# Optimization experiments

Measured on AMD Instinct MI355X. Metric: run time of the kernel, lower is better.

The kernel has to match this reference:

```python
import jax, jax.numpy as jnp
import numpy as np

KERNEL_SIZES = [2, 4, 8, 16, 32, 64]
MAXK = max(k + k // 2 for k in KERNEL_SIZES[1:])  # 96
PAD_LO = (MAXK - 1) // 2  # 47
PAD_HI = MAXK - 1 - PAD_LO  # 48


def _alternating(K, even_negative):
    f = np.ones(K, np.float32)
    idx = np.arange(K)
    mask = (idx % 2 == 0) if even_negative else (idx % 2 == 1)
    f[mask] = -1.0
    return f


def make_weight_bank():
    """Builds all 17 fixed filters, zero-padded and center-aligned into one
    (17, 1, MAXK) bank so a single 'same'-padded conv matches 17 torch convs.
    Alignment: torch pads left=(K-1)//2 for kernel K; embedding each kernel at
    offset (MAXK-1)//2 - (K-1)//2 inside a MAXK kernel padded (PAD_LO, PAD_HI)
    reproduces the identical output."""
    filters = []
    for K in KERNEL_SIZES:              # group 1: -1 at even indices
        filters.append(_alternating(K, True))
    for K in KERNEL_SIZES:              # group 2: -1 at odd indices
        filters.append(_alternating(K, False))
    for K in KERNEL_SIZES[1:]:          # group 3: piecewise quadratic, len K + K//2
        q = K // 4
        left = (np.linspace(0.0, 1.0, q + 1, dtype=np.float32)[1:]) ** 2
        right = left[::-1]
        filters.append(np.concatenate([-left, -right, 2 * left, 2 * right, -left, -right]).astype(np.float32))
    W = np.zeros((len(filters), 1, MAXK), np.float32)
    for i, f in enumerate(filters):
        K = len(f)
        o = (MAXK - 1) // 2 - (K - 1) // 2
        W[i, 0, o:o + K] = f
    return jnp.asarray(W)


def setup_inputs() -> dict:
    key = jax.random.key(0)
    x = jax.random.normal(key, (128, 1, 32768), dtype=jnp.float32)
    W = make_weight_bank()  # (17, 1, 96), fixed non-trainable filters
    return {"x": x, "W": W}


def reference(x, W):
    # x: (B, 1, L); W: (17, 1, MAXK). One cross-correlation conv = bank of 17
    # 'same'-padded conv1d filters; then ReLU.
    y = jax.lax.conv_general_dilated(
        x, W,
        window_strides=(1,),
        padding=[(PAD_LO, PAD_HI)],
        dimension_numbers=("NCH", "OIH", "NCH"),
    )
    return jax.nn.relu(y)  # (B, 17, L)
```

## Files before the change

### kernel.cpp

```cpp
#include <hip/hip_runtime.h>


#define S_LEN    32768
#define NFILT    17
#define TILE     1024
#define NTHREADS 256
#define PITCH    284
#define NCHUNK   139

constexpr int Z4_OFF  = 0;
constexpr int Z8_OFF  = Z4_OFF + TILE + 16;
constexpr int Z16_OFF = Z8_OFF + TILE + 32;
constexpr int ZTOT    = Z16_OFF + TILE + 64;

typedef float fvec4 __attribute__((ext_vector_type(4)));

template<int Qv>
__device__ __forceinline__ float bw(int i) {
    constexpr float inv = 1.0f / (float)Qv;
    const float t = (i < Qv) ? (float)(i + 1) * inv : (float)(2 * Qv - i) * inv;
    return t * t;
}

template<int Qv>
__device__ __forceinline__ float third_w(int j) {
    constexpr float inv = 1.0f / (float)Qv;
    const int seg = j / Qv;
    const int i = j - seg * Qv;
    const float t = ((seg & 1) == 0) ? (float)(i + 1) * inv : (float)(Qv - i) * inv;
    const float v = t * t;
    return (seg == 2 || seg == 3) ? 2.0f * v : -v;
}

template<int Qv>
__device__ __forceinline__ void zcalc(const float* __restrict__ xsl,
                                      float* __restrict__ Zf, int bi) {
    constexpr int OFF  = 49 - 3 * Qv;
    constexpr int A0Q  = OFF >> 2;
    constexpr int SH   = OFF & 3;
    constexpr int SPAN = 2 * Qv;
    constexpr int NW   = (SH + SPAN + 3 + 3) >> 2;
    const float4* __restrict__ xs4 =
        reinterpret_cast<const float4*>(xsl) + bi + A0Q;
    float a0 = 0.f, a1 = 0.f, a2 = 0.f, a3 = 0.f;
#pragma unroll
    for (int wi = 0; wi < NW; ++wi) {
        const float4 xw = xs4[wi];
#pragma unroll
        for (int e = 0; e < 4; ++e) {
            const int u = 4 * wi + e - SH;
            const float xv = (e == 0) ? xw.x : (e == 1) ? xw.y
                           : (e == 2) ? xw.z : xw.w;
            if (u >= 0 && u < SPAN)     a0 = fmaf(bw<Qv>(u),     xv, a0);
            if (u >= 1 && u < SPAN + 1) a1 = fmaf(bw<Qv>(u - 1), xv, a1);
            if (u >= 2 && u < SPAN + 2) a2 = fmaf(bw<Qv>(u - 2), xv, a2);
            if (u >= 3 && u < SPAN + 3) a3 = fmaf(bw<Qv>(u - 3), xv, a3);
        }
    }
    reinterpret_cast<float4*>(Zf)[bi] = make_float4(a0, a1, a2, a3);
}

template<int Qv>
__device__ __forceinline__ float4 bump_out(const float* __restrict__ Zf, int tid) {
    const float4* __restrict__ Z4 = reinterpret_cast<const float4*>(Zf);
    const float4 za = Z4[tid];
    const float4 zb = Z4[tid + (Qv >> 1)];
    const float4 zc = Z4[tid + Qv];
    float4 y;
    y.x = fmaf(2.f, zb.x, -(za.x + zc.x));
    y.y = fmaf(2.f, zb.y, -(za.y + zc.y));
    y.z = fmaf(2.f, zb.z, -(za.z + zc.z));
    y.w = fmaf(2.f, zb.w, -(za.w + zc.w));
    return y;
}

template<int Qv>
__device__ __forceinline__ float4 bump_direct(const float* __restrict__ xsl, int tid) {
    constexpr int SPAN = 6 * Qv;
    constexpr int C    = (SPAN - 1) / 2;
    constexpr int OFF  = 48 - C;
    constexpr int A0   = OFF >> 2;
    constexpr int SH   = OFF & 3;
    constexpr int NW   = (SH + SPAN + 3 + 3) >> 2;
    const float4* __restrict__ xs4 =
        reinterpret_cast<const float4*>(xsl) + tid + A0;
    float a0 = 0.f, a1 = 0.f, a2 = 0.f, a3 = 0.f;
#pragma unroll
    for (int wi = 0; wi < NW; ++wi) {
        const float4 xw = xs4[wi];
#pragma unroll
        for (int e = 0; e < 4; ++e) {
            const int u = 4 * wi + e - SH;
            const float xv = (e == 0) ? xw.x : (e == 1) ? xw.y
                           : (e == 2) ? xw.z : xw.w;
            if (u >= 0 && u < SPAN)     a0 = fmaf(third_w<Qv>(u),     xv, a0);
            if (u >= 1 && u < SPAN + 1) a1 = fmaf(third_w<Qv>(u - 1), xv, a1);
            if (u >= 2 && u < SPAN + 2) a2 = fmaf(third_w<Qv>(u - 2), xv, a2);
            if (u >= 3 && u < SPAN + 3) a3 = fmaf(third_w<Qv>(u - 3), xv, a3);
        }
    }
    return make_float4(a0, a1, a2, a3);
}

__device__ __forceinline__ void alt24_direct(const float* __restrict__ xsl, int tid,
                                             float4& o2, float4& o4) {
    const float4* __restrict__ xs4 =
        reinterpret_cast<const float4*>(xsl) + tid + 11;
    const float4 wA = xs4[0], wB = xs4[1], wC = xs4[2];
    const float s3 = wA.w, s4 = wB.x, s5 = wB.y, s6 = wB.z,
                s7 = wB.w, s8 = wC.x, s9 = wC.y;
    o2.x = s5 - s4;  o2.y = s6 - s5;  o2.z = s7 - s6;  o2.w = s8 - s7;
    o4.x = (s4 - s3) + (s6 - s5);
    o4.y = (s5 - s4) + (s7 - s6);
    o4.z = (s6 - s5) + (s8 - s7);
    o4.w = (s7 - s6) + (s9 - s8);
}

template<int K>
__device__ __forceinline__ float4 alt_acc(const float* __restrict__ Psp, int tid) {
    constexpr int H = (K - 1) / 2;
    float v[4];
#pragma unroll
    for (int r = 0; r < 4; ++r) {
        const int dn  = 48 - H + r;
        const int dn2 = dn + K;
        const float pa = Psp[(dn  & 3) * PITCH + tid + (dn  >> 2)];
        const float pb = Psp[(dn2 & 3) * PITCH + tid + (dn2 >> 2)];
        const float dd = pb - pa;
        v[r] = ((r + H) & 1) ? dd : -dd;
    }
    return make_float4(v[0], v[1], v[2], v[3]);
}

__global__ __launch_bounds__(NTHREADS, 6)
void conv_bank_kernel(const float* __restrict__ x, float* __restrict__ out) {
    __shared__ __align__(16) float xsl[1136];
    __shared__ float Psp[4 * PITCH];
    __shared__ __align__(16) float Zb[ZTOT];
    __shared__ float wtot[2];

    const int tid = threadIdx.x;
    const int bx  = blockIdx.x;
    const int ts  = bx * TILE;
    const int b   = blockIdx.y;
    const float* __restrict__ xrow = x + (size_t)b * S_LEN;

    if (bx >= 1 && bx <= 30) {
        const float4* __restrict__ g4 =
            reinterpret_cast<const float4*>(xrow) + ((ts - 48) >> 2);
        float4* __restrict__ s4 = reinterpret_cast<float4*>(xsl);
#pragma unroll
        for (int i = tid; i < 284; i += NTHREADS)
            s4[i] = (i < 281) ? g4[i] : make_float4(0.f, 0.f, 0.f, 0.f);
    } else {
        for (int j = tid; j < 1136; j += NTHREADS) {
            const int g = ts - 48 + j;
            xsl[j] = (j < 1124 && (unsigned)g < (unsigned)S_LEN) ? xrow[g] : 0.f;
        }
    }
    __syncthreads();

    float4 xa, xb;
    float csum = 0.f, incl;
    {
        const float4* __restrict__ xs4 = reinterpret_cast<const float4*>(xsl);
        if (tid < NCHUNK) {
            xa = xs4[2 * tid];
            xb = xs4[2 * tid + 1];
            csum = (xa.x - xa.y) + (xa.z - xa.w)
                 + (xb.x - xb.y) + (xb.z - xb.w);
        }
        incl = csum;
#pragma unroll
        for (int off = 1; off < 64; off <<= 1) {
            const float v = __shfl_up(incl, off, 64);
            if ((tid & 63) >= off) incl += v;
        }
        if ((tid & 63) == 63 && tid < 128) wtot[tid >> 6] = incl;
    }
    zcalc<16>(xsl, Zb + Z16_OFF, tid);
    zcalc<8 >(xsl, Zb + Z8_OFF,  tid);
    if (tid >= 192 && tid < 208) zcalc<16>(xsl, Zb + Z16_OFF, 256 + (tid - 192));
    if (tid >= 208 && tid < 216) zcalc<8 >(xsl, Zb + Z8_OFF,  256 + (tid - 208));
    __syncthreads();

    const int t0 = ts + 4 * tid;
    float* __restrict__ obase = out + (size_t)b * (NFILT * S_LEN) + t0;

    auto store_relu = [&](int j, float4 v) {
        fvec4 s;
        s.x = fmaxf(v.x, 0.f); s.y = fmaxf(v.y, 0.f);
        s.z = fmaxf(v.z, 0.f); s.w = fmaxf(v.w, 0.f);
        __builtin_nontemporal_store(
            s, reinterpret_cast<fvec4*>(obase + (size_t)j * S_LEN));
    };
    auto store_pair = [&](int j, float4 a) {
        store_relu(j, a);
        store_relu(j + 6, make_float4(-a.x, -a.y, -a.z, -a.w));
    };

    store_relu(16, bump_out<16>(Zb + Z16_OFF, tid));
    store_relu(15, bump_out<8 >(Zb + Z8_OFF,  tid));
    store_relu(12, bump_direct<1>(xsl, tid));
    store_relu(13, bump_direct<2>(xsl, tid));
    {
        float4 a2, a4;
        alt24_direct(xsl, tid, a2, a4);
        store_pair(0, a2);
        store_pair(1, a4);
    }

    zcalc<4>(xsl, Zb + Z4_OFF, tid);
    if (tid >= 216 && tid < 220) zcalc<4>(xsl, Zb + Z4_OFF, 256 + (tid - 216));

    if (tid < NCHUNK) {
        float offs = (tid >= 64) ? wtot[0] : 0.f;
        if (tid >= 128) offs += wtot[1];
        float run = offs + (incl - csum);
        float* __restrict__ Pb = Psp + 2 * tid;
        Pb[0 * PITCH + 0] = run; run += xa.x;
        Pb[1 * PITCH + 0] = run; run -= xa.y;
        Pb[2 * PITCH + 0] = run; run += xa.z;
        Pb[3 * PITCH + 0] = run; run -= xa.w;
        Pb[0 * PITCH + 1] = run; run += xb.x;
        Pb[1 * PITCH + 1] = run; run -= xb.y;
        Pb[2 * PITCH + 1] = run; run += xb.z;
        Pb[3 * PITCH + 1] = run;
    }

    asm volatile("s_waitcnt lgkmcnt(0)" ::: "memory");
    __builtin_amdgcn_s_barrier();

    store_pair(2, alt_acc<8 >(Psp, tid));
    store_pair(3, alt_acc<16>(Psp, tid));
    store_pair(4, alt_acc<32>(Psp, tid));
    store_pair(5, alt_acc<64>(Psp, tid));
    store_relu(14, bump_out<4>(Zb + Z4_OFF, tid));
}

extern "C" void kernel_launch(void* const* d_in, const int* in_sizes, int n_in,
                              void* d_out, int out_size, void* d_ws, size_t ws_size,
                              hipStream_t stream) {
    const float* x = (const float*)d_in[0];
    float* out = (float*)d_out;
    const int nbatch = in_sizes[0] / S_LEN;
    dim3 grid(S_LEN / TILE, nbatch, 1);
    conv_bank_kernel<<<grid, NTHREADS, 0, stream>>>(x, out);
}
```

Before: 297.8 us.

## Split work per output filter with per-block sequential tiles and prefetch

Reassigns each block to a single output filter and half a row, looping over 16 tiles with register-staged prefetch of the next input tile, instead of one block computing all 17 filters for one tile. Blocks are mapped so that blocks on the same XCD share batch rows, for L2 reuse of the input. The aim is that each output channel is written as one long contiguous stream and that per-block shared memory and registers shrink to raise occupancy. In exchange, every input tile is reloaded and recomputed (prefix scans, Z sums) by up to 17 blocks, the batch size is hardcoded, and each tile iteration adds extra barriers.

```diff
diff --git a/kernel.cpp b/kernel.cpp
--- a/kernel.cpp
+++ b/kernel.cpp
@@ -2,16 +2,11 @@
 
 
 #define S_LEN    32768
-#define NFILT    17
+#define NTHREADS 256
 #define TILE     1024
-#define NTHREADS 256
+#define NCHK     16
 #define PITCH    284
-#define NCHUNK   139
-
-constexpr int Z4_OFF  = 0;
-constexpr int Z8_OFF  = Z4_OFF + TILE + 16;
-constexpr int Z16_OFF = Z8_OFF + TILE + 32;
-constexpr int ZTOT    = Z16_OFF + TILE + 64;
+#define NSCAN    139
 
 typedef float fvec4 __attribute__((ext_vector_type(4)));
 
@@ -21,7 +16,6 @@
     const float t = (i < Qv) ? (float)(i + 1) * inv : (float)(2 * Qv - i) * inv;
     return t * t;
 }
-
 template<int Qv>
 __device__ __forceinline__ float third_w(int j) {
     constexpr float inv = 1.0f / (float)Qv;
@@ -30,6 +24,35 @@
     const float t = ((seg & 1) == 0) ? (float)(i + 1) * inv : (float)(Qv - i) * inv;
     const float v = t * t;
     return (seg == 2 || seg == 3) ? 2.0f * v : -v;
+}
+
+struct StageRegs { float4 a, b; };
+
+__device__ __forceinline__ float4 guarded_ld(const float4* __restrict__ g4, int w) {
+    if ((unsigned)w < (unsigned)(S_LEN / 4)) return g4[w];
+    return make_float4(0.f, 0.f, 0.f, 0.f);
+}
+__device__ __forceinline__ StageRegs stage_load(const float4* __restrict__ g4,
+                                                int ts, int tid) {
+    const int wb = (ts >> 2) - 12;
+    StageRegs r;
+    r.a = guarded_ld(g4, wb + tid);
+    r.b = (tid < 24) ? guarded_ld(g4, wb + 256 + tid)
+                     : make_float4(0.f, 0.f, 0.f, 0.f);
+    return r;
+}
+__device__ __forceinline__ void stage_write(float* __restrict__ xsl,
+                                            const StageRegs& r, int tid) {
+    float4* s4 = reinterpret_cast<float4*>(xsl);
+    s4[tid] = r.a;
+    if (tid < 24) s4[256 + tid] = r.b;
+}
+
+__device__ __forceinline__ void store_relu(float* __restrict__ p, float4 v) {
+    fvec4 s;
+    s.x = fmaxf(v.x, 0.f); s.y = fmaxf(v.y, 0.f);
+    s.z = fmaxf(v.z, 0.f); s.w = fmaxf(v.w, 0.f);
+    __builtin_nontemporal_store(s, reinterpret_cast<fvec4*>(p));
 }
 
 template<int Qv>
@@ -102,20 +125,6 @@
     return make_float4(a0, a1, a2, a3);
 }
 
-__device__ __forceinline__ void alt24_direct(const float* __restrict__ xsl, int tid,
-                                             float4& o2, float4& o4) {
-    const float4* __restrict__ xs4 =
-        reinterpret_cast<const float4*>(xsl) + tid + 11;
-    const float4 wA = xs4[0], wB = xs4[1], wC = xs4[2];
-    const float s3 = wA.w, s4 = wB.x, s5 = wB.y, s6 = wB.z,
-                s7 = wB.w, s8 = wC.x, s9 = wC.y;
-    o2.x = s5 - s4;  o2.y = s6 - s5;  o2.z = s7 - s6;  o2.w = s8 - s7;
-    o4.x = (s4 - s3) + (s6 - s5);
-    o4.y = (s5 - s4) + (s7 - s6);
-    o4.z = (s6 - s5) + (s8 - s7);
-    o4.w = (s7 - s6) + (s9 - s8);
-}
-
 template<int K>
 __device__ __forceinline__ float4 alt_acc(const float* __restrict__ Psp, int tid) {
     constexpr int H = (K - 1) / 2;
@@ -132,110 +141,132 @@
     return make_float4(v[0], v[1], v[2], v[3]);
 }
 
-__global__ __launch_bounds__(NTHREADS, 6)
-void conv_bank_kernel(const float* __restrict__ x, float* __restrict__ out) {
-    __shared__ __align__(16) float xsl[1136];
-    __shared__ float Psp[4 * PITCH];
-    __shared__ __align__(16) float Zb[ZTOT];
-    __shared__ float wtot[2];
-
-    const int tid = threadIdx.x;
-    const int bx  = blockIdx.x;
-    const int ts  = bx * TILE;
-    const int b   = blockIdx.y;
-    const float* __restrict__ xrow = x + (size_t)b * S_LEN;
-
-    if (bx >= 1 && bx <= 30) {
-        const float4* __restrict__ g4 =
-            reinterpret_cast<const float4*>(xrow) + ((ts - 48) >> 2);
-        float4* __restrict__ s4 = reinterpret_cast<float4*>(xsl);
-#pragma unroll
-        for (int i = tid; i < 284; i += NTHREADS)
-            s4[i] = (i < 281) ? g4[i] : make_float4(0.f, 0.f, 0.f, 0.f);
-    } else {
-        for (int j = tid; j < 1136; j += NTHREADS) {
-            const int g = ts - 48 + j;
-            xsl[j] = (j < 1124 && (unsigned)g < (unsigned)S_LEN) ? xrow[g] : 0.f;
-        }
-    }
-    __syncthreads();
-
-    float4 xa, xb;
-    float csum = 0.f, incl;
-    {
-        const float4* __restrict__ xs4 = reinterpret_cast<const float4*>(xsl);
-        if (tid < NCHUNK) {
-            xa = xs4[2 * tid];
-            xb = xs4[2 * tid + 1];
+template<int K, bool NEG>
+__device__ __forceinline__ void run_alt(const float4* __restrict__ g4,
+                                        float* __restrict__ smem,
+                                        float* __restrict__ outp,
+                                        int tbase, int tid) {
+    float* xsl  = smem;
+    float* Psp  = smem + 1120;
+    float* wtot = smem + 1120 + 1136;
+    const float4* xs4 = reinterpret_cast<const float4*>(xsl);
+
+    StageRegs nxt = stage_load(g4, tbase, tid);
+    stage_write(xsl, nxt, tid);
+    for (int c = 0; c < NCHK; ++c) {
+        __syncthreads();
+        if (c + 1 < NCHK) nxt = stage_load(g4, tbase + (c + 1) * TILE, tid);
+        float4 xa, xb; float csum = 0.f;
+        if (tid < NSCAN) {
+            xa = xs4[2 * tid]; xb = xs4[2 * tid + 1];
             csum = (xa.x - xa.y) + (xa.z - xa.w)
                  + (xb.x - xb.y) + (xb.z - xb.w);
         }
-        incl = csum;
+        float incl = csum;
 #pragma unroll
         for (int off = 1; off < 64; off <<= 1) {
             const float v = __shfl_up(incl, off, 64);
             if ((tid & 63) >= off) incl += v;
         }
         if ((tid & 63) == 63 && tid < 128) wtot[tid >> 6] = incl;
-    }
-    zcalc<16>(xsl, Zb + Z16_OFF, tid);
-    zcalc<8 >(xsl, Zb + Z8_OFF,  tid);
-    if (tid >= 192 && tid < 208) zcalc<16>(xsl, Zb + Z16_OFF, 256 + (tid - 192));
-    if (tid >= 208 && tid < 216) zcalc<8 >(xsl, Zb + Z8_OFF,  256 + (tid - 208));
-    __syncthreads();
-
-    const int t0 = ts + 4 * tid;
-    float* __restrict__ obase = out + (size_t)b * (NFILT * S_LEN) + t0;
-
-    auto store_relu = [&](int j, float4 v) {
-        fvec4 s;
-        s.x = fmaxf(v.x, 0.f); s.y = fmaxf(v.y, 0.f);
-        s.z = fmaxf(v.z, 0.f); s.w = fmaxf(v.w, 0.f);
-        __builtin_nontemporal_store(
-            s, reinterpret_cast<fvec4*>(obase + (size_t)j * S_LEN));
-    };
-    auto store_pair = [&](int j, float4 a) {
-        store_relu(j, a);
-        store_relu(j + 6, make_float4(-a.x, -a.y, -a.z, -a.w));
-    };
-
-    store_relu(16, bump_out<16>(Zb + Z16_OFF, tid));
-    store_relu(15, bump_out<8 >(Zb + Z8_OFF,  tid));
-    store_relu(12, bump_direct<1>(xsl, tid));
-    store_relu(13, bump_direct<2>(xsl, tid));
-    {
-        float4 a2, a4;
-        alt24_direct(xsl, tid, a2, a4);
-        store_pair(0, a2);
-        store_pair(1, a4);
-    }
-
-    zcalc<4>(xsl, Zb + Z4_OFF, tid);
-    if (tid >= 216 && tid < 220) zcalc<4>(xsl, Zb + Z4_OFF, 256 + (tid - 216));
-
-    if (tid < NCHUNK) {
-        float offs = (tid >= 64) ? wtot[0] : 0.f;
-        if (tid >= 128) offs += wtot[1];
-        float run = offs + (incl - csum);
-        float* __restrict__ Pb = Psp + 2 * tid;
-        Pb[0 * PITCH + 0] = run; run += xa.x;
-        Pb[1 * PITCH + 0] = run; run -= xa.y;
-        Pb[2 * PITCH + 0] = run; run += xa.z;
-        Pb[3 * PITCH + 0] = run; run -= xa.w;
-        Pb[0 * PITCH + 1] = run; run += xb.x;
-        Pb[1 * PITCH + 1] = run; run -= xb.y;
-        Pb[2 * PITCH + 1] = run; run += xb.z;
-        Pb[3 * PITCH + 1] = run;
-    }
-
-    asm volatile("s_waitcnt lgkmcnt(0)" ::: "memory");
-    __builtin_amdgcn_s_barrier();
-
-    store_pair(2, alt_acc<8 >(Psp, tid));
-    store_pair(3, alt_acc<16>(Psp, tid));
-    store_pair(4, alt_acc<32>(Psp, tid));
-    store_pair(5, alt_acc<64>(Psp, tid));
-    store_relu(14, bump_out<4>(Zb + Z4_OFF, tid));
+        __syncthreads();
+        if (c + 1 < NCHK) stage_write(xsl, nxt, tid);
+        if (tid < NSCAN) {
+            float offs = (tid >= 64) ? wtot[0] : 0.f;
+            if (tid >= 128) offs += wtot[1];
+            float run = offs + (incl - csum);
+            float* Pb = Psp + 2 * tid;
+            Pb[0 * PITCH + 0] = run; run += xa.x;
+            Pb[1 * PITCH + 0] = run; run -= xa.y;
+            Pb[2 * PITCH + 0] = run; run += xa.z;
+            Pb[3 * PITCH + 0] = run; run -= xa.w;
+            Pb[0 * PITCH + 1] = run; run += xb.x;
+            Pb[1 * PITCH + 1] = run; run -= xb.y;
+            Pb[2 * PITCH + 1] = run; run += xb.z;
+            Pb[3 * PITCH + 1] = run;
+        }
+        __syncthreads();
+        float4 v = alt_acc<K>(Psp, tid);
+        if (NEG) { v.x = -v.x; v.y = -v.y; v.z = -v.z; v.w = -v.w; }
+        store_relu(outp + tbase + c * TILE, v);
+    }
+}
+
+template<int Qv>
+__device__ __forceinline__ void run_bumpZ(const float4* __restrict__ g4,
+                                          float* __restrict__ smem,
+                                          float* __restrict__ outp,
+                                          int tbase, int tid) {
+    float* xsl = smem;
+    float* Zb  = smem + 1120;
+    StageRegs nxt = stage_load(g4, tbase, tid);
+    stage_write(xsl, nxt, tid);
+    for (int c = 0; c < NCHK; ++c) {
+        __syncthreads();
+        if (c + 1 < NCHK) nxt = stage_load(g4, tbase + (c + 1) * TILE, tid);
+        zcalc<Qv>(xsl, Zb, tid);
+        if (tid >= NTHREADS - Qv)
+            zcalc<Qv>(xsl, Zb, 256 + (tid - (NTHREADS - Qv)));
+        __syncthreads();
+        if (c + 1 < NCHK) stage_write(xsl, nxt, tid);
+        store_relu(outp + tbase + c * TILE, bump_out<Qv>(Zb, tid));
+    }
+}
+
+template<int Qv>
+__device__ __forceinline__ void run_bumpD(const float4* __restrict__ g4,
+                                          float* __restrict__ smem,
+                                          float* __restrict__ outp,
+                                          int tbase, int tid) {
+    float* xsl = smem;
+    StageRegs nxt = stage_load(g4, tbase, tid);
+    stage_write(xsl, nxt, tid);
+    for (int c = 0; c < NCHK; ++c) {
+        __syncthreads();
+        if (c + 1 < NCHK) nxt = stage_load(g4, tbase + (c + 1) * TILE, tid);
+        const float4 y = bump_direct<Qv>(xsl, tid);
+        __syncthreads();
+        if (c + 1 < NCHK) stage_write(xsl, nxt, tid);
+        store_relu(outp + tbase + c * TILE, y);
+    }
+}
+
+__global__ __launch_bounds__(NTHREADS, 8)
+void conv_bank_kernel(const float* __restrict__ x, float* __restrict__ out) {
+    __shared__ __align__(16) float smem[1120 + 1136 + 2];
+
+    const int tid = threadIdx.x;
+    const int g   = blockIdx.x;
+    const int xcd = g & 7;
+    const int i   = g >> 3;
+    const int bi  = i / 34;
+    const int r   = i - bi * 34;
+    const int b   = xcd * 16 + bi;
+    const int j   = r >> 1;
+    const int tbase = (r & 1) * (S_LEN / 2);
+
+    const float4* g4 = reinterpret_cast<const float4*>(x + (size_t)b * S_LEN);
+    float* outp = out + ((size_t)b * 17 + j) * S_LEN + 4 * tid;
+
+    switch (j) {
+    case 0:  run_alt<2,  false>(g4, smem, outp, tbase, tid); break;
+    case 1:  run_alt<4,  false>(g4, smem, outp, tbase, tid); break;
+    case 2:  run_alt<8,  false>(g4, smem, outp, tbase, tid); break;
+    case 3:  run_alt<16, false>(g4, smem, outp, tbase, tid); break;
+    case 4:  run_alt<32, false>(g4, smem, outp, tbase, tid); break;
+    case 5:  run_alt<64, false>(g4, smem, outp, tbase, tid); break;
+    case 6:  run_alt<2,  true >(g4, smem, outp, tbase, tid); break;
+    case 7:  run_alt<4,  true >(g4, smem, outp, tbase, tid); break;
+    case 8:  run_alt<8,  true >(g4, smem, outp, tbase, tid); break;
+    case 9:  run_alt<16, true >(g4, smem, outp, tbase, tid); break;
+    case 10: run_alt<32, true >(g4, smem, outp, tbase, tid); break;
+    case 11: run_alt<64, true >(g4, smem, outp, tbase, tid); break;
+    case 12: run_bumpD<1 >(g4, smem, outp, tbase, tid); break;
+    case 13: run_bumpD<2 >(g4, smem, outp, tbase, tid); break;
+    case 14: run_bumpZ<4 >(g4, smem, outp, tbase, tid); break;
+    case 15: run_bumpZ<8 >(g4, smem, outp, tbase, tid); break;
+    case 16: run_bumpZ<16>(g4, smem, outp, tbase, tid); break;
+    }
 }
 
 extern "C" void kernel_launch(void* const* d_in, const int* in_sizes, int n_in,
@@ -243,7 +274,7 @@
                               hipStream_t stream) {
     const float* x = (const float*)d_in[0];
     float* out = (float*)d_out;
-    const int nbatch = in_sizes[0] / S_LEN;
-    dim3 grid(S_LEN / TILE, nbatch, 1);
+    (void)in_sizes; (void)n_in; (void)d_ws; (void)ws_size; (void)out_size;
+    dim3 grid(128 * 17 * 2, 1, 1);
     conv_bank_kernel<<<grid, NTHREADS, 0, stream>>>(x, out);
 }
```

Result: slower. 339.0 us (+13.8%).
